# Optimization experiments

Hardware: AMD Instinct MI355X
Metric: run time of the kernel (lower is better)

The kernel has to match this reference:

```python
import jax, jax.numpy as jnp
import numpy as np

EPS = 1e-5  # torch BatchNorm1d default eps
CATAGORY = 2


def setup_inputs() -> dict:
    key = jax.random.key(0)
    ks = jax.random.split(key, 8)
    B, N, D, P = 64, 512, 512, 720
    return {
        "x": jax.random.normal(ks[0], (B, N, D), dtype=jnp.float32),
        "W_exp": jax.random.normal(ks[1], (CATAGORY, D, P), dtype=jnp.float32) * 0.02,
        "b_exp": jax.random.normal(ks[2], (CATAGORY, P), dtype=jnp.float32) * 0.02,
        "W1": jax.random.normal(ks[3], (D, 128), dtype=jnp.float32) * 0.05,
        "b1": jnp.zeros((128,), jnp.float32),
        "g1": jnp.ones((128,), jnp.float32),
        "be1": jnp.zeros((128,), jnp.float32),
        "m1": jnp.zeros((128,), jnp.float32),
        "v1": jnp.ones((128,), jnp.float32),
        "W2": jax.random.normal(ks[4], (128, 32), dtype=jnp.float32) * 0.1,
        "b2": jnp.zeros((32,), jnp.float32),
        "g2": jnp.ones((32,), jnp.float32),
        "be2": jnp.zeros((32,), jnp.float32),
        "m2": jnp.zeros((32,), jnp.float32),
        "v2": jnp.ones((32,), jnp.float32),
        "W3": jax.random.normal(ks[5], (32, 1), dtype=jnp.float32) * 0.1,
        "b3": jnp.zeros((1,), jnp.float32),
    }


def _bn(h, gamma, beta, mean, var):
    # BatchNorm1d, eval mode (running stats); dropout is identity in eval
    return (h - mean) * jax.lax.rsqrt(var + EPS) * gamma + beta


def reference(x, W_exp, b_exp, W1, b1, g1, be1, m1, v1,
              W2, b2, g2, be2, m2, v2, W3, b3):
    B, N, D = x.shape
    xf = x.reshape(B * N, D)
    # classifier: Linear -> BN -> ReLU -> Linear -> BN -> ReLU -> Linear -> Sigmoid
    h = jax.nn.relu(_bn(xf @ W1 + b1, g1, be1, m1, v1))
    h = jax.nn.relu(_bn(h @ W2 + b2, g2, be2, m2, v2))
    z = jax.nn.sigmoid(h @ W3 + b3).reshape(B, N)  # [B, N] class score
    # per-token expert index (sigmoid score rounded to {0, 1})
    idx = jnp.clip(jnp.round(z), 0, CATAGORY - 1).astype(jnp.int32)  # [B, N]
    # compute all experts (catagory=2, cheap) then gather per-token choice
    outs = jnp.einsum("bnd,edp->bnep", x, W_exp) + b_exp  # [B, N, E, P]
    sel = jnp.take_along_axis(outs, idx[:, :, None, None], axis=2)
    return sel[:, :, 0, :]  # [B, N, pred_len]
```

## Files before the change

### kernel.cpp

```cpp
#include <hip/hip_runtime.h>

#define DEV __device__ __forceinline__

typedef __bf16 bf16x8 __attribute__((ext_vector_type(8)));
typedef float f32x4 __attribute__((ext_vector_type(4)));
typedef float f32x2 __attribute__((ext_vector_type(2)));

constexpr int TOK = 32768;
constexpr int D   = 512;
constexpr int P   = 720;
constexpr float EPS = 1e-5f;

DEV unsigned short f2bf(float f) {
  unsigned u = __float_as_uint(f);
  u += 0x7FFFu + ((u >> 16) & 1u);
  return (unsigned short)(u >> 16);
}

DEV void g2lds16(const void* g, void* l) {
  __builtin_amdgcn_global_load_lds(
      (__attribute__((address_space(1))) void*)g,
      (__attribute__((address_space(3))) void*)l, 16, 0, 0);
}

__global__ void wconv_kernel(const float* __restrict__ W,
                             unsigned short* __restrict__ WT) {
  __shared__ float ls[16][17];
  const int e  = blockIdx.z;
  const int d0 = blockIdx.x * 16, p0 = blockIdx.y * 16;
  const int tx = threadIdx.x, ty = threadIdx.y;
  ls[ty][tx] = W[((size_t)e * D + d0 + ty) * P + p0 + tx];
  __syncthreads();
  WT[((size_t)e * P + p0 + ty) * D + d0 + tx] = f2bf(ls[tx][ty]);
}

__global__ __launch_bounds__(256, 3) void classifier_kernel(
    const float* __restrict__ x,
    const float* __restrict__ W1, const float* __restrict__ b1,
    const float* __restrict__ g1, const float* __restrict__ be1,
    const float* __restrict__ m1, const float* __restrict__ v1,
    const float* __restrict__ W2, const float* __restrict__ b2,
    const float* __restrict__ g2, const float* __restrict__ be2,
    const float* __restrict__ m2, const float* __restrict__ v2,
    const float* __restrict__ W3, const float* __restrict__ b3,
    unsigned short* __restrict__ xb, unsigned long long* __restrict__ masks)
{
  constexpr int TM = 64, BK = 32;
  __shared__ __align__(16) char smem[50176];
  float (*xs)[32][68]  = (float(*)[32][68])smem;
  float (*ws)[32][128] = (float(*)[32][128])(smem + 17408);
  float (*h1s)[68]     = (float(*)[68])smem;
  float (*h2s)[68]     = (float(*)[68])(smem + 34816);

  const int tid  = threadIdx.x;
  const int wave = tid >> 6;
  const int lane = tid & 63;
  const int t0   = blockIdx.x * TM;

  const int xr = tid >> 2;
  const int xc = (tid & 3) * 4;

  const int kb = (tid >> 7) * 16;
  const int th = tid & 127;
  const int tg = th >> 4;
  const int cg = th & 15;

  float acc[8][8];
  #pragma unroll
  for (int i = 0; i < 8; ++i)
    #pragma unroll
    for (int j = 0; j < 8; ++j) acc[i][j] = 0.f;

  float4 px0, px1;

  auto issue_x = [&](int kt) {
    const float* base = &x[(size_t)(t0 + xr) * D + kt * BK + xc];
    px0 = *reinterpret_cast<const float4*>(base);
    px1 = *reinterpret_cast<const float4*>(base + 16);
  };
  auto commit_x = [&](int b, int kt) {
    xs[b][xc + 0][xr] = px0.x;  xs[b][xc + 1][xr] = px0.y;
    xs[b][xc + 2][xr] = px0.z;  xs[b][xc + 3][xr] = px0.w;
    xs[b][xc + 16][xr] = px1.x; xs[b][xc + 17][xr] = px1.y;
    xs[b][xc + 18][xr] = px1.z; xs[b][xc + 19][xr] = px1.w;
    ushort4 u0, u1;
    u0.x = f2bf(px0.x); u0.y = f2bf(px0.y); u0.z = f2bf(px0.z); u0.w = f2bf(px0.w);
    u1.x = f2bf(px1.x); u1.y = f2bf(px1.y); u1.z = f2bf(px1.z); u1.w = f2bf(px1.w);
    unsigned short* xbase = &xb[(size_t)(t0 + xr) * D + kt * BK + xc];
    *reinterpret_cast<ushort4*>(xbase)      = u0;
    *reinterpret_cast<ushort4*>(xbase + 16) = u1;
  };
  auto issue_w = [&](int b, int kt) {
    char* ldsbase = (char*)&ws[b][0][0];
    const int kk = (lane >> 5);
    const int ch = (lane & 31) * 4;
    #pragma unroll
    for (int i = 0; i < 4; ++i) {
      const int op = wave * 4 + i;
      g2lds16(&W1[(size_t)(kt * BK + op * 2 + kk) * 128 + ch],
              (char*)ldsbase + op * 1024);
    }
  };

  issue_w(0, 0);
  issue_x(0);
  commit_x(0, 0);
  __syncthreads();

  int buf = 0;
  for (int kt = 0; kt < D / BK; ++kt) {
    const int nb = buf ^ 1;
    if (kt < D / BK - 1) {
      issue_w(nb, kt + 1);
      issue_x(kt + 1);
    }
    #pragma unroll 8
    for (int kk = 0; kk < 16; ++kk) {
      const int kr = kb + kk;
      const f32x4 xa  = *reinterpret_cast<const f32x4*>(&xs[buf][kr][tg * 8]);
      const f32x4 xv2 = *reinterpret_cast<const f32x4*>(&xs[buf][kr][tg * 8 + 4]);
      const f32x4 wa  = *reinterpret_cast<const f32x4*>(&ws[buf][kr][cg * 4]);
      const f32x4 wb  = *reinterpret_cast<const f32x4*>(&ws[buf][kr][64 + cg * 4]);
      const float xr8[8] = {xa[0], xa[1], xa[2], xa[3],
                            xv2[0], xv2[1], xv2[2], xv2[3]};
      const float wr8[8] = {wa[0], wa[1], wa[2], wa[3],
                            wb[0], wb[1], wb[2], wb[3]};
      #pragma unroll
      for (int i = 0; i < 8; ++i)
        #pragma unroll
        for (int j = 0; j < 8; ++j)
          acc[i][j] = fmaf(xr8[i], wr8[j], acc[i][j]);
    }
    if (kt < D / BK - 1) commit_x(nb, kt + 1);
    __syncthreads();
    buf = nb;
  }

  if (kb) {
    #pragma unroll
    for (int j = 0; j < 8; ++j) {
      const int col = (j < 4) ? (cg * 4 + j) : (60 + cg * 4 + j);
      float4 p0 = {acc[0][j], acc[1][j], acc[2][j], acc[3][j]};
      float4 p1 = {acc[4][j], acc[5][j], acc[6][j], acc[7][j]};
      *reinterpret_cast<float4*>(&h1s[col][tg * 8])     = p0;
      *reinterpret_cast<float4*>(&h1s[col][tg * 8 + 4]) = p1;
    }
  }
  __syncthreads();
  if (!kb) {
    #pragma unroll
    for (int j = 0; j < 8; ++j) {
      const int col = (j < 4) ? (cg * 4 + j) : (60 + cg * 4 + j);
      const float4 q0 = *reinterpret_cast<const float4*>(&h1s[col][tg * 8]);
      const float4 q1 = *reinterpret_cast<const float4*>(&h1s[col][tg * 8 + 4]);
      const float A  = g1[col] / sqrtf(v1[col] + EPS);
      const float Bc = (b1[col] - m1[col]) * A + be1[col];
      float4 h0, h1v;
      h0.x = fmaxf(0.f, fmaf(acc[0][j] + q0.x, A, Bc));
      h0.y = fmaxf(0.f, fmaf(acc[1][j] + q0.y, A, Bc));
      h0.z = fmaxf(0.f, fmaf(acc[2][j] + q0.z, A, Bc));
      h0.w = fmaxf(0.f, fmaf(acc[3][j] + q0.w, A, Bc));
      h1v.x = fmaxf(0.f, fmaf(acc[4][j] + q1.x, A, Bc));
      h1v.y = fmaxf(0.f, fmaf(acc[5][j] + q1.y, A, Bc));
      h1v.z = fmaxf(0.f, fmaf(acc[6][j] + q1.z, A, Bc));
      h1v.w = fmaxf(0.f, fmaf(acc[7][j] + q1.w, A, Bc));
      *reinterpret_cast<float4*>(&h1s[col][tg * 8])     = h0;
      *reinterpret_cast<float4*>(&h1s[col][tg * 8 + 4]) = h1v;
    }
  }
  __syncthreads();

  {
    const int c2 = (tid & 7) * 4;
    const int t2 = (tid >> 3) * 2;
    f32x2 a2[4];
    #pragma unroll
    for (int c = 0; c < 4; ++c) a2[c] = (f32x2)0.f;
    #pragma unroll 8
    for (int j = 0; j < 128; ++j) {
      const f32x2 h = *reinterpret_cast<const f32x2*>(&h1s[j][t2]);
      const float4 w = *reinterpret_cast<const float4*>(&W2[j * 32 + c2]);
      const float wr[4] = {w.x, w.y, w.z, w.w};
      #pragma unroll
      for (int c = 0; c < 4; ++c) {
        f32x2 wv = {wr[c], wr[c]};
        a2[c] = __builtin_elementwise_fma(h, wv, a2[c]);
      }
    }
    #pragma unroll
    for (int c = 0; c < 4; ++c) {
      const int col = c2 + c;
      const float A  = g2[col] / sqrtf(v2[col] + EPS);
      const float Bc = (b2[col] - m2[col]) * A + be2[col];
      f32x2 hv;
      hv[0] = fmaxf(0.f, fmaf(a2[c][0], A, Bc));
      hv[1] = fmaxf(0.f, fmaf(a2[c][1], A, Bc));
      *reinterpret_cast<f32x2*>(&h2s[col][t2]) = hv;
    }
  }
  __syncthreads();

  if (tid < TM) {
    float logit = b3[0];
    #pragma unroll
    for (int k = 0; k < 32; ++k)
      logit = fmaf(h2s[k][tid], W3[k], logit);
    unsigned long long m = __ballot(logit > 0.f);
    if (tid == 0) masks[blockIdx.x] = m;
  }
}

__global__ __launch_bounds__(512) void scan_kernel(
    const unsigned long long* __restrict__ masks,
    int* __restrict__ off1s)
{
  __shared__ int s[512];
  const int t = threadIdx.x;
  const int c1 = __popcll(masks[t]);
  s[t] = c1;
  __syncthreads();
  #pragma unroll
  for (int d = 1; d < 512; d <<= 1) {
    int v = (t >= d) ? s[t - d] : 0;
    __syncthreads();
    s[t] += v;
    __syncthreads();
  }
  off1s[t] = s[t] - c1;
  if (t == 511) off1s[512] = s[511];
}

__global__ __launch_bounds__(256) void scatter_kernel(
    const unsigned long long* __restrict__ masks,
    const int* __restrict__ off1s,
    int* __restrict__ lists)
{
  const int wave = threadIdx.x >> 6;
  const int lane = threadIdx.x & 63;
  const int b = blockIdx.x * 4 + wave;
  const unsigned long long m = masks[b];
  const int off1 = off1s[b];
  const int off0 = b * 64 - off1;
  const int r1 = __popcll(m & ((1ull << lane) - 1ull));
  const int r0 = lane - r1;
  const int tok = b * 64 + lane;
  if ((m >> lane) & 1ull) lists[TOK + off1 + r1] = tok;
  else                    lists[off0 + r0] = tok;
}

__global__ __launch_bounds__(256) void expert_gemm_kernel(
    const unsigned short* __restrict__ xb,
    const unsigned short* __restrict__ WT,
    const float* __restrict__ b_exp,
    const int* __restrict__ off1s,
    const int* __restrict__ lists,
    float* __restrict__ out)
{
  constexpr int GM = 128, GN = 144, GK = 32;
  constexpr int NT = D / GK;
  __shared__ __align__(16) unsigned short As[4][GM * GK];
  __shared__ __align__(16) unsigned short Bs[4][GN * GK];

  const int tid  = threadIdx.x;
  const int wave = tid >> 6;
  const int lane = tid & 63;

  const int n1 = off1s[512];
  const int n0 = TOK - n1;
  const int T0 = (n0 + GM - 1) >> 7;
  const int T1 = (n1 + GM - 1) >> 7;

  const int wg    = blockIdx.x;
  const int xcd   = wg & 7;
  const int local = wg >> 3;
  const int gt    = xcd * 33 + local / 5;
  const int pt    = local % 5;
  if (gt >= T0 + T1) return;
  const int e  = (gt >= T0) ? 1 : 0;
  const int ne = e ? n1 : n0;
  const int m0 = (e ? gt - T0 : gt) * GM;
  const int p0 = pt * GN;
  const int* lst = lists + e * TOK;

  const int col  = lane & 15;
  const int rg   = lane >> 4;
  const int srow = lane >> 2;
  const int sswz = (lane & 3) ^ ((srow >> 1) & 3);

  int aid[2];
  #pragma unroll
  for (int i = 0; i < 2; ++i) {
    const int r = (wave + i * 4) * 16 + srow;
    int g = m0 + r; if (g > ne - 1) g = ne - 1;
    aid[i] = lst[g];
  }
  int eid[2][4]; unsigned evalid = 0;
  #pragma unroll
  for (int mf = 0; mf < 2; ++mf)
    #pragma unroll
    for (int j = 0; j < 4; ++j) {
      const int g = m0 + wave * 32 + mf * 16 + rg * 4 + j;
      const int gc = (g > ne - 1) ? ne - 1 : g;
      eid[mf][j] = lst[gc];
      if (g < ne) evalid |= 1u << (mf * 4 + j);
    }
  float be[9];
  #pragma unroll
  for (int nf = 0; nf < 9; ++nf)
    be[nf] = b_exp[e * P + p0 + nf * 16 + col];
  asm volatile("s_waitcnt vmcnt(0)" ::: "memory");

  f32x4 acc[2][9];
  #pragma unroll
  for (int mf = 0; mf < 2; ++mf)
    #pragma unroll
    for (int nf = 0; nf < 9; ++nf) acc[mf][nf] = (f32x4)(0.f);

  auto stage = [&](int b, int kt) {
    const int k0 = kt * GK;
    #pragma unroll
    for (int i = 0; i < 2; ++i) {
      const int c = wave + i * 4;
      g2lds16(xb + (size_t)aid[i] * D + k0 + sswz * 8,
              (char*)As[b] + c * 1024);
    }
    #pragma unroll
    for (int i = 0; i < 3; ++i) {
      const int c = wave + i * 4;
      if (c < 9) {
        const int pr = c * 16 + srow;
        g2lds16(WT + ((size_t)e * P + p0 + pr) * D + k0 + sswz * 8,
                (char*)Bs[b] + c * 1024);
      }
    }
  };

  stage(0, 0);
  stage(1, 1);
  stage(2, 2);

  #pragma unroll
  for (int kt = 0; kt < NT; ++kt) {
    if (kt < NT - 2) {
      if (wave == 0) asm volatile("s_waitcnt vmcnt(10)" ::: "memory");
      else           asm volatile("s_waitcnt vmcnt(8)"  ::: "memory");
    } else if (kt == NT - 2) {
      if (wave == 0) asm volatile("s_waitcnt vmcnt(5)" ::: "memory");
      else           asm volatile("s_waitcnt vmcnt(4)" ::: "memory");
    } else {
      asm volatile("s_waitcnt vmcnt(0)" ::: "memory");
    }
    __builtin_amdgcn_s_barrier();
    __builtin_amdgcn_sched_barrier(0);

    if (kt + 3 < NT) stage((kt + 3) & 3, kt + 3);

    const int buf = kt & 3;
    bf16x8 af[2];
    #pragma unroll
    for (int mf = 0; mf < 2; ++mf) {
      const int r  = wave * 32 + mf * 16 + (lane & 15);
      const int ch = (lane >> 4) ^ ((r >> 1) & 3);
      af[mf] = *(const bf16x8*)((const char*)As[buf] + r * 64 + ch * 16);
    }
    #pragma unroll
    for (int nf = 0; nf < 9; ++nf) {
      const int pr = nf * 16 + (lane & 15);
      const int ch = (lane >> 4) ^ ((pr >> 1) & 3);
      bf16x8 bfrag = *(const bf16x8*)((const char*)Bs[buf] + pr * 64 + ch * 16);
      #pragma unroll
      for (int mf = 0; mf < 2; ++mf)
        acc[mf][nf] = __builtin_amdgcn_mfma_f32_16x16x32_bf16(
            af[mf], bfrag, acc[mf][nf], 0, 0, 0);
    }
  }

  #pragma unroll
  for (int nf = 0; nf < 9; ++nf) {
    const int p = p0 + nf * 16 + col;
    #pragma unroll
    for (int mf = 0; mf < 2; ++mf) {
      #pragma unroll
      for (int j = 0; j < 4; ++j) {
        if (evalid & (1u << (mf * 4 + j)))
          out[(size_t)eid[mf][j] * P + p] = acc[mf][nf][j] + be[nf];
      }
    }
  }
}

extern "C" void kernel_launch(void* const* d_in, const int* in_sizes, int n_in,
                              void* d_out, int out_size, void* d_ws, size_t ws_size,
                              hipStream_t stream) {
  const float* x     = (const float*)d_in[0];
  const float* W_exp = (const float*)d_in[1];
  const float* b_exp = (const float*)d_in[2];
  const float* W1 = (const float*)d_in[3];
  const float* b1 = (const float*)d_in[4];
  const float* g1 = (const float*)d_in[5];
  const float* be1 = (const float*)d_in[6];
  const float* m1 = (const float*)d_in[7];
  const float* v1 = (const float*)d_in[8];
  const float* W2 = (const float*)d_in[9];
  const float* b2 = (const float*)d_in[10];
  const float* g2 = (const float*)d_in[11];
  const float* be2 = (const float*)d_in[12];
  const float* m2 = (const float*)d_in[13];
  const float* v2 = (const float*)d_in[14];
  const float* W3 = (const float*)d_in[15];
  const float* b3 = (const float*)d_in[16];
  float* out = (float*)d_out;

  char* wsb = (char*)d_ws;
  unsigned short* xb = (unsigned short*)wsb;
  unsigned short* WT = (unsigned short*)(wsb + 33554432);
  unsigned long long* masks = (unsigned long long*)(wsb + 35028992);
  int* off1s = (int*)(wsb + 35033088);
  int* lists = (int*)(wsb + 35036160);

  hipLaunchKernelGGL(wconv_kernel, dim3(D / 16, P / 16, 2), dim3(16, 16),
                     0, stream, W_exp, WT);
  hipLaunchKernelGGL(classifier_kernel, dim3(TOK / 64), dim3(256), 0, stream,
                     x, W1, b1, g1, be1, m1, v1, W2, b2, g2, be2, m2, v2, W3, b3,
                     xb, masks);
  hipLaunchKernelGGL(scan_kernel, dim3(1), dim3(512), 0, stream, masks, off1s);
  hipLaunchKernelGGL(scatter_kernel, dim3(128), dim3(256), 0, stream,
                     masks, off1s, lists);
  hipLaunchKernelGGL(expert_gemm_kernel, dim3(8 * 33 * 5), dim3(256),
                     0, stream, xb, WT, b_exp, off1s, lists, out);
}
```

Before: 124.5 us.

## Split classifier K-loop across four thread groups with 512-thread blocks

The classifier kernel now uses 512 threads per block and splits each 32-wide K tile into four 8-row slices instead of two 16-row slices. Each thread loads one float4 of x per tile rather than two, and issues half as many W1 global-to-LDS copies. The partial accumulators are reduced through shared memory in three serialized steps with extra barriers. This aims to raise occupancy and latency hiding in the first-layer GEMM, at the cost of more reduction traffic and synchronisation, and with only half the threads active in the second-layer stage.

```diff
diff --git a/kernel.cpp b/kernel.cpp
--- a/kernel.cpp
+++ b/kernel.cpp
@@ -34,7 +34,7 @@
   WT[((size_t)e * P + p0 + ty) * D + d0 + tx] = f2bf(ls[tx][ty]);
 }
 
-__global__ __launch_bounds__(256, 3) void classifier_kernel(
+__global__ __launch_bounds__(512, 4) void classifier_kernel(
     const float* __restrict__ x,
     const float* __restrict__ W1, const float* __restrict__ b1,
     const float* __restrict__ g1, const float* __restrict__ be1,
@@ -57,10 +57,11 @@
   const int lane = tid & 63;
   const int t0   = blockIdx.x * TM;
 
-  const int xr = tid >> 2;
-  const int xc = (tid & 3) * 4;
-
-  const int kb = (tid >> 7) * 16;
+  const int xr = tid >> 3;
+  const int xc = (tid & 7) * 4;
+
+  const int kq = tid >> 7;
+  const int kb = kq * 8;
   const int th = tid & 127;
   const int tg = th >> 4;
   const int cg = th & 15;
@@ -71,32 +72,25 @@
     #pragma unroll
     for (int j = 0; j < 8; ++j) acc[i][j] = 0.f;
 
-  float4 px0, px1;
+  float4 px0;
 
   auto issue_x = [&](int kt) {
-    const float* base = &x[(size_t)(t0 + xr) * D + kt * BK + xc];
-    px0 = *reinterpret_cast<const float4*>(base);
-    px1 = *reinterpret_cast<const float4*>(base + 16);
+    px0 = *reinterpret_cast<const float4*>(&x[(size_t)(t0 + xr) * D + kt * BK + xc]);
   };
   auto commit_x = [&](int b, int kt) {
     xs[b][xc + 0][xr] = px0.x;  xs[b][xc + 1][xr] = px0.y;
     xs[b][xc + 2][xr] = px0.z;  xs[b][xc + 3][xr] = px0.w;
-    xs[b][xc + 16][xr] = px1.x; xs[b][xc + 17][xr] = px1.y;
-    xs[b][xc + 18][xr] = px1.z; xs[b][xc + 19][xr] = px1.w;
-    ushort4 u0, u1;
+    ushort4 u0;
     u0.x = f2bf(px0.x); u0.y = f2bf(px0.y); u0.z = f2bf(px0.z); u0.w = f2bf(px0.w);
-    u1.x = f2bf(px1.x); u1.y = f2bf(px1.y); u1.z = f2bf(px1.z); u1.w = f2bf(px1.w);
-    unsigned short* xbase = &xb[(size_t)(t0 + xr) * D + kt * BK + xc];
-    *reinterpret_cast<ushort4*>(xbase)      = u0;
-    *reinterpret_cast<ushort4*>(xbase + 16) = u1;
+    *reinterpret_cast<ushort4*>(&xb[(size_t)(t0 + xr) * D + kt * BK + xc]) = u0;
   };
   auto issue_w = [&](int b, int kt) {
     char* ldsbase = (char*)&ws[b][0][0];
     const int kk = (lane >> 5);
     const int ch = (lane & 31) * 4;
     #pragma unroll
-    for (int i = 0; i < 4; ++i) {
-      const int op = wave * 4 + i;
+    for (int i = 0; i < 2; ++i) {
+      const int op = wave * 2 + i;
       g2lds16(&W1[(size_t)(kt * BK + op * 2 + kk) * 128 + ch],
               (char*)ldsbase + op * 1024);
     }
@@ -114,8 +108,8 @@
       issue_w(nb, kt + 1);
       issue_x(kt + 1);
     }
-    #pragma unroll 8
-    for (int kk = 0; kk < 16; ++kk) {
+    #pragma unroll 4
+    for (int kk = 0; kk < 8; ++kk) {
       const int kr = kb + kk;
       const f32x4 xa  = *reinterpret_cast<const f32x4*>(&xs[buf][kr][tg * 8]);
       const f32x4 xv2 = *reinterpret_cast<const f32x4*>(&xs[buf][kr][tg * 8 + 4]);
@@ -136,7 +130,7 @@
     buf = nb;
   }
 
-  if (kb) {
+  if (kq == 3) {
     #pragma unroll
     for (int j = 0; j < 8; ++j) {
       const int col = (j < 4) ? (cg * 4 + j) : (60 + cg * 4 + j);
@@ -147,7 +141,23 @@
     }
   }
   __syncthreads();
-  if (!kb) {
+  #pragma unroll 1
+  for (int q = 2; q >= 1; --q) {
+    if (kq == q) {
+      #pragma unroll
+      for (int j = 0; j < 8; ++j) {
+        const int col = (j < 4) ? (cg * 4 + j) : (60 + cg * 4 + j);
+        float4 q0 = *reinterpret_cast<const float4*>(&h1s[col][tg * 8]);
+        float4 q1 = *reinterpret_cast<const float4*>(&h1s[col][tg * 8 + 4]);
+        q0.x += acc[0][j]; q0.y += acc[1][j]; q0.z += acc[2][j]; q0.w += acc[3][j];
+        q1.x += acc[4][j]; q1.y += acc[5][j]; q1.z += acc[6][j]; q1.w += acc[7][j];
+        *reinterpret_cast<float4*>(&h1s[col][tg * 8])     = q0;
+        *reinterpret_cast<float4*>(&h1s[col][tg * 8 + 4]) = q1;
+      }
+    }
+    __syncthreads();
+  }
+  if (kq == 0) {
     #pragma unroll
     for (int j = 0; j < 8; ++j) {
       const int col = (j < 4) ? (cg * 4 + j) : (60 + cg * 4 + j);
@@ -170,7 +180,7 @@
   }
   __syncthreads();
 
-  {
+  if (tid < 256) {
     const int c2 = (tid & 7) * 4;
     const int t2 = (tid >> 3) * 2;
     f32x2 a2[4];
@@ -420,7 +430,7 @@
 
   hipLaunchKernelGGL(wconv_kernel, dim3(D / 16, P / 16, 2), dim3(16, 16),
                      0, stream, W_exp, WT);
-  hipLaunchKernelGGL(classifier_kernel, dim3(TOK / 64), dim3(256), 0, stream,
+  hipLaunchKernelGGL(classifier_kernel, dim3(TOK / 64), dim3(512), 0, stream,
                      x, W1, b1, g1, be1, m1, v1, W2, b2, g2, be2, m2, v2, W3, b3,
                      xb, masks);
   hipLaunchKernelGGL(scan_kernel, dim3(1), dim3(512), 0, stream, masks, off1s);
```

Measured after the change: 152.0 us. 22.1% more time.

## Restructure classifier GEMM to wave-uniform W1 columns read via scalar loads

Applied to the files above, without the earlier changes.

The first classifier layer is reorganised so each wave owns 32 output columns and each lane owns one token. W1 is then read directly from global memory at a wave-uniform address, letting the compiler use scalar loads, instead of being staged through LDS with async copies. This removes the W1 LDS buffer, the split-K reduction through shared memory and one barrier, and shrinks LDS use. In exchange each thread does one LDS read per k for 32 FMAs, with much less register-level reuse than the old 8x8 outer product, and W1 traffic now depends on the scalar cache.

```diff
diff --git a/kernel.cpp b/kernel.cpp
--- a/kernel.cpp
+++ b/kernel.cpp
@@ -46,30 +46,26 @@
     unsigned short* __restrict__ xb, unsigned long long* __restrict__ masks)
 {
   constexpr int TM = 64, BK = 32;
-  __shared__ __align__(16) char smem[50176];
-  float (*xs)[32][68]  = (float(*)[32][68])smem;
-  float (*ws)[32][128] = (float(*)[32][128])(smem + 17408);
-  float (*h1s)[68]     = (float(*)[68])smem;
-  float (*h2s)[68]     = (float(*)[68])(smem + 34816);
+  __shared__ __align__(16) char smem[43520];
+  float (*xs)[32][68] = (float(*)[32][68])smem;
+  float (*h1s)[68]    = (float(*)[68])smem;
+  float (*h2s)[68]    = (float(*)[68])(smem + 34816);
 
   const int tid  = threadIdx.x;
-  const int wave = tid >> 6;
   const int lane = tid & 63;
   const int t0   = blockIdx.x * TM;
 
+  const int wv = __builtin_amdgcn_readfirstlane(tid >> 6);
+  const int c0 = wv * 32;
+
   const int xr = tid >> 2;
   const int xc = (tid & 3) * 4;
 
-  const int kb = (tid >> 7) * 16;
-  const int th = tid & 127;
-  const int tg = th >> 4;
-  const int cg = th & 15;
-
-  float acc[8][8];
-  #pragma unroll
-  for (int i = 0; i < 8; ++i)
-    #pragma unroll
-    for (int j = 0; j < 8; ++j) acc[i][j] = 0.f;
+  const int tt = lane;
+
+  float acc[32];
+  #pragma unroll
+  for (int j = 0; j < 32; ++j) acc[j] = 0.f;
 
   float4 px0, px1;
 
@@ -90,19 +86,7 @@
     *reinterpret_cast<ushort4*>(xbase)      = u0;
     *reinterpret_cast<ushort4*>(xbase + 16) = u1;
   };
-  auto issue_w = [&](int b, int kt) {
-    char* ldsbase = (char*)&ws[b][0][0];
-    const int kk = (lane >> 5);
-    const int ch = (lane & 31) * 4;
-    #pragma unroll
-    for (int i = 0; i < 4; ++i) {
-      const int op = wave * 4 + i;
-      g2lds16(&W1[(size_t)(kt * BK + op * 2 + kk) * 128 + ch],
-              (char*)ldsbase + op * 1024);
-    }
-  };
-
-  issue_w(0, 0);
+
   issue_x(0);
   commit_x(0, 0);
   __syncthreads();
@@ -110,63 +94,27 @@
   int buf = 0;
   for (int kt = 0; kt < D / BK; ++kt) {
     const int nb = buf ^ 1;
-    if (kt < D / BK - 1) {
-      issue_w(nb, kt + 1);
-      issue_x(kt + 1);
-    }
-    #pragma unroll 8
-    for (int kk = 0; kk < 16; ++kk) {
-      const int kr = kb + kk;
-      const f32x4 xa  = *reinterpret_cast<const f32x4*>(&xs[buf][kr][tg * 8]);
-      const f32x4 xv2 = *reinterpret_cast<const f32x4*>(&xs[buf][kr][tg * 8 + 4]);
-      const f32x4 wa  = *reinterpret_cast<const f32x4*>(&ws[buf][kr][cg * 4]);
-      const f32x4 wb  = *reinterpret_cast<const f32x4*>(&ws[buf][kr][64 + cg * 4]);
-      const float xr8[8] = {xa[0], xa[1], xa[2], xa[3],
-                            xv2[0], xv2[1], xv2[2], xv2[3]};
-      const float wr8[8] = {wa[0], wa[1], wa[2], wa[3],
-                            wb[0], wb[1], wb[2], wb[3]};
+    if (kt < D / BK - 1) issue_x(kt + 1);
+    const float* wtile = W1 + (size_t)(kt * BK) * 128 + c0;
+    #pragma unroll 4
+    for (int kk = 0; kk < BK; ++kk) {
+      const float xv = xs[buf][kk][tt];
+      const float* wrow = wtile + (size_t)kk * 128;
       #pragma unroll
-      for (int i = 0; i < 8; ++i)
-        #pragma unroll
-        for (int j = 0; j < 8; ++j)
-          acc[i][j] = fmaf(xr8[i], wr8[j], acc[i][j]);
+      for (int j = 0; j < 32; ++j)
+        acc[j] = fmaf(wrow[j], xv, acc[j]);
     }
     if (kt < D / BK - 1) commit_x(nb, kt + 1);
     __syncthreads();
     buf = nb;
   }
 
-  if (kb) {
-    #pragma unroll
-    for (int j = 0; j < 8; ++j) {
-      const int col = (j < 4) ? (cg * 4 + j) : (60 + cg * 4 + j);
-      float4 p0 = {acc[0][j], acc[1][j], acc[2][j], acc[3][j]};
-      float4 p1 = {acc[4][j], acc[5][j], acc[6][j], acc[7][j]};
-      *reinterpret_cast<float4*>(&h1s[col][tg * 8])     = p0;
-      *reinterpret_cast<float4*>(&h1s[col][tg * 8 + 4]) = p1;
-    }
-  }
-  __syncthreads();
-  if (!kb) {
-    #pragma unroll
-    for (int j = 0; j < 8; ++j) {
-      const int col = (j < 4) ? (cg * 4 + j) : (60 + cg * 4 + j);
-      const float4 q0 = *reinterpret_cast<const float4*>(&h1s[col][tg * 8]);
-      const float4 q1 = *reinterpret_cast<const float4*>(&h1s[col][tg * 8 + 4]);
-      const float A  = g1[col] / sqrtf(v1[col] + EPS);
-      const float Bc = (b1[col] - m1[col]) * A + be1[col];
-      float4 h0, h1v;
-      h0.x = fmaxf(0.f, fmaf(acc[0][j] + q0.x, A, Bc));
-      h0.y = fmaxf(0.f, fmaf(acc[1][j] + q0.y, A, Bc));
-      h0.z = fmaxf(0.f, fmaf(acc[2][j] + q0.z, A, Bc));
-      h0.w = fmaxf(0.f, fmaf(acc[3][j] + q0.w, A, Bc));
-      h1v.x = fmaxf(0.f, fmaf(acc[4][j] + q1.x, A, Bc));
-      h1v.y = fmaxf(0.f, fmaf(acc[5][j] + q1.y, A, Bc));
-      h1v.z = fmaxf(0.f, fmaf(acc[6][j] + q1.z, A, Bc));
-      h1v.w = fmaxf(0.f, fmaf(acc[7][j] + q1.w, A, Bc));
-      *reinterpret_cast<float4*>(&h1s[col][tg * 8])     = h0;
-      *reinterpret_cast<float4*>(&h1s[col][tg * 8 + 4]) = h1v;
-    }
+  #pragma unroll 4
+  for (int j = 0; j < 32; ++j) {
+    const int col = c0 + j;
+    const float A  = g1[col] / sqrtf(v1[col] + EPS);
+    const float Bc = (b1[col] - m1[col]) * A + be1[col];
+    h1s[col][tt] = fmaxf(0.f, fmaf(acc[j], A, Bc));
   }
   __syncthreads();
 
@@ -183,8 +131,8 @@
       const float wr[4] = {w.x, w.y, w.z, w.w};
       #pragma unroll
       for (int c = 0; c < 4; ++c) {
-        f32x2 wv = {wr[c], wr[c]};
-        a2[c] = __builtin_elementwise_fma(h, wv, a2[c]);
+        f32x2 wv2 = {wr[c], wr[c]};
+        a2[c] = __builtin_elementwise_fma(h, wv2, a2[c]);
       }
     }
     #pragma unroll
```

Measured after the change: 204.9 us. 1.65x slower.
